# Kernel tuning notes

Measured on AMD Instinct MI355X. Metric: run time of the kernel, lower is better.

The kernel has to match this reference:

```python
import jax, jax.numpy as jnp
import numpy as np

N, E, DIN, H, EIN, EH, STEPS = 10000, 100000, 64, 64, 16, 128, 3


def setup_inputs() -> dict:
    key = jax.random.key(0)
    ks = jax.random.split(key, 8)
    n_feat = jax.random.normal(ks[0], (N, DIN), jnp.float32)
    e_feat = jax.random.normal(ks[1], (E, EIN), jnp.float32)
    src = jax.random.randint(ks[2], (E,), 0, N, jnp.int32)
    dst = jax.random.randint(ks[3], (E,), 0, N, jnp.int32)
    W0 = jax.random.normal(ks[4], (DIN, H), jnp.float32) / np.sqrt(DIN)
    b0 = jnp.zeros((H,), jnp.float32)
    We1 = jax.random.normal(ks[5], (EIN, EH), jnp.float32) / np.sqrt(EIN)
    be1 = jnp.zeros((EH,), jnp.float32)
    # small scale so per-edge HxH weight matrices keep activations stable
    We2 = jax.random.normal(ks[6], (EH, H * H), jnp.float32) * 0.02
    be2 = jnp.zeros((H * H,), jnp.float32)
    conv_bias = jnp.zeros((H,), jnp.float32)
    gamma = jnp.ones((H,), jnp.float32)
    beta = jnp.zeros((H,), jnp.float32)
    return {"n_feat": n_feat, "e_feat": e_feat, "src": src, "dst": dst,
            "W0": W0, "b0": b0, "We1": We1, "be1": be1, "We2": We2,
            "be2": be2, "conv_bias": conv_bias, "gamma": gamma, "beta": beta}


def reference(n_feat, e_feat, src, dst, W0, b0, We1, be1, We2, be2, conv_bias, gamma, beta):
    n = n_feat.shape[0]
    h = W0.shape[1]
    out = jax.nn.relu(n_feat @ W0 + b0)  # [N,H]
    # edge network (eval mode: dropout = identity); e_feat is fixed so the
    # per-edge weight matrices are identical each step -> compute once.
    w_edge = (jax.nn.relu(e_feat @ We1 + be1) @ We2 + be2).reshape(-1, h, h)  # [E,H,H]
    for _ in range(STEPS):
        msg = jnp.einsum('ei,eio->eo', out[src], w_edge)  # gather + per-edge matmul
        agg = jax.ops.segment_sum(msg, dst, num_segments=n)  # scatter-sum to dst
        out = jax.nn.relu(agg + conv_bias)
    # BatchNorm1d over nodes (training-mode batch statistics)
    mean = jnp.mean(out, axis=0)
    var = jnp.var(out, axis=0)
    return (out - mean) * jax.lax.rsqrt(var + 1e-5) * gamma + beta
```

## Files before the change

### kernel.cpp

```cpp
#include <hip/hip_runtime.h>
#include <stdint.h>

#define DIN   64
#define HDIM  64
#define EIN   16
#define EHID  128
#define HH    4096
#define TC    8256
#define STEPS 3

typedef short bf16x8 __attribute__((ext_vector_type(8)));
typedef float f32x4  __attribute__((ext_vector_type(4)));

__device__ __forceinline__ unsigned short f32_to_bf16(float f) {
    union { float f; uint32_t u; } v; v.f = f;
    uint32_t r = v.u + 0x7fffu + ((v.u >> 16) & 1u);
    return (unsigned short)(r >> 16);
}
__device__ __forceinline__ float bfu_to_f(unsigned short u) {
    union { uint32_t u; float f; } v; v.u = (uint32_t)u << 16; return v.f;
}

__global__ void k_node_mlp(const float* __restrict__ nf, const float* __restrict__ W0,
                           const float* __restrict__ b0, float* __restrict__ outb,
                           unsigned short* __restrict__ outbf, int n_nodes) {
    __shared__ float w0s[DIN * HDIM];
    int tid = threadIdx.x;
    for (int i = tid; i < DIN * HDIM; i += 256) w0s[i] = W0[i];
    __syncthreads();
    int node = blockIdx.x * 4 + (tid >> 6);
    int o = tid & 63;
    if (node >= n_nodes) return;
    float xr = nf[node * DIN + o];
    float acc = b0[o];
#pragma unroll 8
    for (int i = 0; i < DIN; ++i)
        acc += __shfl(xr, i, 64) * w0s[i * HDIM + o];
    float v = fmaxf(acc, 0.f);
    outb[node * HDIM + o] = v;
    outbf[node * HDIM + o] = f32_to_bf16(v);
}

__global__ void k_edge_mlp(const float* __restrict__ ef, const float* __restrict__ We1,
                           const float* __restrict__ be1, unsigned short* __restrict__ h, int n_edges) {
    int tid = threadIdx.x;
    int e = blockIdx.x * 2 + (tid >> 7);
    int c = tid & 127;
    if (e >= n_edges) return;
    float acc = be1[c];
    const float* x = ef + (size_t)e * EIN;
#pragma unroll
    for (int i = 0; i < EIN; ++i) acc += x[i] * We1[i * EHID + c];
    h[(size_t)e * EHID + c] = f32_to_bf16(fmaxf(acc, 0.f));
}

__global__ void k_bmat(const float* __restrict__ We2, const float* __restrict__ be2,
                       unsigned short* __restrict__ BmatT) {
    int t = blockIdx.x * 256 + threadIdx.x;
    if (t >= TC * 64) return;
    int c = t >> 6, i = t & 63;
    int g = c & 63;
    int m = (c & ~63) + 4 * (g & 15) + (g >> 4);
    float v;
    if (m < 8192) {
        int k = ((m >> 11) << 5) | (m & 31);
        int o = (m >> 5) & 63;
        v = We2[k * HH + i * 64 + o];
    } else {
        v = be2[i * 64 + (m - 8192)];
    }
    BmatT[t] = f32_to_bf16(v);
}

__global__ void k_T(const unsigned short* __restrict__ outbf, const unsigned short* __restrict__ BmatT,
                    unsigned short* __restrict__ T, int n0, int n1) {
    int wave = threadIdx.x >> 6, lane = threadIdx.x & 63;
    int r = lane & 15, q = lane >> 4;
    int eb = n0 + blockIdx.y * 64;
    int cb = blockIdx.x * 256 + wave * 64;
    f32x4 acc[4][4] = {};
#pragma unroll
    for (int s = 0; s < 2; ++s) {
        bf16x8 afr[4], bfr[4];
#pragma unroll
        for (int mt = 0; mt < 4; ++mt) {
            int e = eb + mt * 16 + r;
            if (e >= n1) e = n1 - 1;
            afr[mt] = *(const bf16x8*)(outbf + (size_t)e * 64 + s * 32 + q * 8);
        }
#pragma unroll
        for (int nt = 0; nt < 4; ++nt) {
            int c = cb + nt * 16 + r;
            if (c >= TC) c = 0;
            bfr[nt] = *(const bf16x8*)(BmatT + (size_t)c * 64 + s * 32 + q * 8);
        }
#pragma unroll
        for (int mt = 0; mt < 4; ++mt)
#pragma unroll
            for (int nt = 0; nt < 4; ++nt)
                acc[mt][nt] = __builtin_amdgcn_mfma_f32_16x16x32_bf16(afr[mt], bfr[nt], acc[mt][nt], 0, 0, 0);
    }
    if (cb >= TC) return;
#pragma unroll
    for (int mt = 0; mt < 4; ++mt)
#pragma unroll
        for (int rg = 0; rg < 4; ++rg) {
            int n = eb + mt * 16 + q * 4 + rg;
            if (n >= n1) continue;
            ushort4 pk;
            pk.x = f32_to_bf16(acc[mt][0][rg]);
            pk.y = f32_to_bf16(acc[mt][1][rg]);
            pk.z = f32_to_bf16(acc[mt][2][rg]);
            pk.w = f32_to_bf16(acc[mt][3][rg]);
            *(ushort4*)(T + (size_t)(n - n0) * TC + cb + 4 * r) = pk;
        }
}

__global__ void k_hist(const int* __restrict__ src, const int* __restrict__ dst,
                       int* __restrict__ cntS, int* __restrict__ cntD, int n_edges) {
    int e = blockIdx.x * 256 + threadIdx.x;
    if (e >= n_edges) return;
    atomicAdd(&cntS[src[e]], 1);
    atomicAdd(&cntD[dst[e]], 1);
}

__global__ void k_scan(const int* __restrict__ cntS, const int* __restrict__ cntD,
                       int* __restrict__ offS, int* __restrict__ offD,
                       int* __restrict__ curS, int* __restrict__ curD, int n, int total) {
    const int* cnt = blockIdx.x ? cntD : cntS;
    int* off = blockIdx.x ? offD : offS;
    int* cur = blockIdx.x ? curD : curS;
    __shared__ int part[256];
    int tid = threadIdx.x;
    int chunk = (n + 255) / 256;
    int c0 = tid * chunk, c1 = c0 + chunk; if (c1 > n) c1 = n; if (c0 > n) c0 = n;
    int s = 0;
    for (int i = c0; i < c1; ++i) s += cnt[i];
    part[tid] = s;
    __syncthreads();
    for (int st = 1; st < 256; st <<= 1) {
        int v = (tid >= st) ? part[tid - st] : 0;
        __syncthreads();
        part[tid] += v;
        __syncthreads();
    }
    int run = tid ? part[tid - 1] : 0;
    for (int i = c0; i < c1; ++i) { off[i] = run; cur[i] = run; run += cnt[i]; }
    if (tid == 0) off[n] = total;
}

__global__ void k_perm(const int* __restrict__ src, const int* __restrict__ dst,
                       int* __restrict__ curS, int* __restrict__ curD,
                       int* __restrict__ permS, int* __restrict__ permD, int n_edges) {
    int e = blockIdx.x * 256 + threadIdx.x;
    if (e >= n_edges) return;
    permS[atomicAdd(&curS[src[e]], 1)] = e;
    permD[atomicAdd(&curD[dst[e]], 1)] = e;
}

__global__ void k_msg(const unsigned short* __restrict__ h, const unsigned short* __restrict__ T,
                      const int* __restrict__ offS, const int* __restrict__ permS,
                      float* __restrict__ msg, int n0, int n1) {
    int wave = threadIdx.x >> 6, lane = threadIdx.x & 63;
    int n = n0 + blockIdx.x * 4 + wave;
    if (n >= n1) return;
    int beg = offS[n], end = offS[n + 1];
    if (beg == end) return;
    int r = lane & 15, q = lane >> 4;
    const unsigned short* Tb = T + (size_t)(n - n0) * TC;
    float bias[4];
#pragma unroll
    for (int nt = 0; nt < 4; ++nt)
        bias[nt] = bfu_to_f(Tb[8192 + nt * 16 + r]);
    for (int j0 = beg; j0 < end; j0 += 16) {
        int jc = j0 + r; if (jc >= end) jc = end - 1;
        int e = permS[jc];
        const unsigned short* he = h + (size_t)e * EHID;
        f32x4 acc[4] = {};
#pragma unroll
        for (int s = 0; s < 4; ++s) {
            bf16x8 afr = *(const bf16x8*)(he + s * 32 + q * 8);
#pragma unroll
            for (int nt = 0; nt < 4; ++nt) {
                bf16x8 bfr = *(const bf16x8*)(Tb + s * 2048 + (nt * 16 + r) * 32 + q * 8);
                acc[nt] = __builtin_amdgcn_mfma_f32_16x16x32_bf16(afr, bfr, acc[nt], 0, 0, 0);
            }
        }
#pragma unroll
        for (int rg = 0; rg < 4; ++rg) {
            int jr = j0 + q * 4 + rg;
            if (jr >= end) continue;
            int er = permS[jr];
#pragma unroll
            for (int nt = 0; nt < 4; ++nt)
                msg[(size_t)er * 64 + nt * 16 + r] = acc[nt][rg] + bias[nt];
        }
    }
}

__global__ void k_agg(const float* __restrict__ msg, const int* __restrict__ offD,
                      const int* __restrict__ permD, const float* __restrict__ cbias,
                      float* __restrict__ outb, unsigned short* __restrict__ outbf, int n_nodes) {
    int wave = threadIdx.x >> 6, lane = threadIdx.x & 63;
    int d = blockIdx.x * 4 + wave;
    if (d >= n_nodes) return;
    float acc = 0.f;
    int end = offD[d + 1];
    for (int j = offD[d]; j < end; ++j)
        acc += msg[(size_t)permD[j] * 64 + lane];
    float v = fmaxf(acc + cbias[lane], 0.f);
    outb[(size_t)d * 64 + lane] = v;
    outbf[(size_t)d * 64 + lane] = f32_to_bf16(v);
}

__global__ void k_bn_stats(const float* __restrict__ out, float* __restrict__ stat, int n_nodes) {
    __shared__ float s1[256], s2[256];
    int tid = threadIdx.x;
    int f = tid & 63, g = tid >> 6;
    float sum = 0.f, ss = 0.f;
    for (int r = blockIdx.x * 4 + g; r < n_nodes; r += 256) {
        float v = out[r * HDIM + f];
        sum += v; ss += v * v;
    }
    s1[tid] = sum; s2[tid] = ss;
    __syncthreads();
    if (tid < 64) {
        float A = s1[tid] + s1[64 + tid] + s1[128 + tid] + s1[192 + tid];
        float B = s2[tid] + s2[64 + tid] + s2[128 + tid] + s2[192 + tid];
        atomicAdd(&stat[tid], A);
        atomicAdd(&stat[64 + tid], B);
    }
}

__global__ void k_bn_final(const float* __restrict__ stat, const float* __restrict__ gamma,
                           const float* __restrict__ beta, float* __restrict__ sc, int n_nodes) {
    int f = threadIdx.x;
    if (f >= 64) return;
    float mean = stat[f] / n_nodes;
    float var  = stat[64 + f] / n_nodes - mean * mean;
    float inv  = rsqrtf(var + 1e-5f);
    float scale = gamma[f] * inv;
    sc[f] = scale;
    sc[64 + f] = beta[f] - mean * scale;
}

__global__ void k_bn_apply(const float* __restrict__ out, const float* __restrict__ sc,
                           float* __restrict__ y, int n) {
    int t = blockIdx.x * 256 + threadIdx.x;
    if (t >= n) return;
    int f = t & 63;
    y[t] = out[t] * sc[f] + sc[64 + f];
}

extern "C" void kernel_launch(void* const* d_in, const int* in_sizes, int n_in,
                              void* d_out, int out_size, void* d_ws, size_t ws_size,
                              hipStream_t stream) {
    const float* nf    = (const float*)d_in[0];
    const float* ef    = (const float*)d_in[1];
    const int*   src   = (const int*)d_in[2];
    const int*   dst   = (const int*)d_in[3];
    const float* W0    = (const float*)d_in[4];
    const float* b0    = (const float*)d_in[5];
    const float* We1   = (const float*)d_in[6];
    const float* be1   = (const float*)d_in[7];
    const float* We2   = (const float*)d_in[8];
    const float* be2   = (const float*)d_in[9];
    const float* cbias = (const float*)d_in[10];
    const float* gamma = (const float*)d_in[11];
    const float* beta  = (const float*)d_in[12];
    (void)n_in; (void)out_size;

    int n_nodes = in_sizes[0] / DIN;
    int n_edges = in_sizes[2];

    char* ws = (char*)d_ws;
    size_t off = 0;
    auto carve = [&](size_t bytes) -> void* {
        void* p = ws + off;
        off = (off + bytes + 255) & ~(size_t)255;
        return p;
    };
    unsigned short* h     = (unsigned short*)carve((size_t)n_edges * EHID * 2);
    float*          msg   = (float*)carve((size_t)n_edges * 64 * 4);
    float*          outb  = (float*)carve((size_t)n_nodes * HDIM * 4);
    unsigned short* outbf = (unsigned short*)carve((size_t)n_nodes * HDIM * 2);
    unsigned short* BmatT = (unsigned short*)carve((size_t)TC * 64 * 2);
    int*            offS  = (int*)carve((size_t)(n_nodes + 1) * 4);
    int*            offD  = (int*)carve((size_t)(n_nodes + 1) * 4);
    int*            curS  = (int*)carve((size_t)n_nodes * 4);
    int*            curD  = (int*)carve((size_t)n_nodes * 4);
    int*            permS = (int*)carve((size_t)n_edges * 4);
    int*            permD = (int*)carve((size_t)n_edges * 4);
    float*          stat  = (float*)carve(128 * 4 + (size_t)2 * n_nodes * 4);
    int*            cntS  = (int*)(stat + 128);
    int*            cntD  = cntS + n_nodes;
    float*          sc    = (float*)carve(128 * 4);
    unsigned short* T     = (unsigned short*)(ws + off);
    size_t avail = ws_size > off ? ws_size - off : 0;
    long tcap = (long)(avail / ((size_t)TC * 2));
    if (tcap > n_nodes) tcap = n_nodes;
    if (tcap < 64) tcap = 64;

    hipMemsetAsync(stat, 0, 128 * 4 + (size_t)2 * n_nodes * 4, stream);

    k_node_mlp<<<dim3((n_nodes + 3) / 4), 256, 0, stream>>>(nf, W0, b0, outb, outbf, n_nodes);
    k_edge_mlp<<<dim3((n_edges + 1) / 2), 256, 0, stream>>>(ef, We1, be1, h, n_edges);
    k_bmat<<<dim3((TC * 64 + 255) / 256), 256, 0, stream>>>(We2, be2, BmatT);
    k_hist<<<dim3((n_edges + 255) / 256), 256, 0, stream>>>(src, dst, cntS, cntD, n_edges);
    k_scan<<<dim3(2), 256, 0, stream>>>(cntS, cntD, offS, offD, curS, curD, n_nodes, n_edges);
    k_perm<<<dim3((n_edges + 255) / 256), 256, 0, stream>>>(src, dst, curS, curD, permS, permD, n_edges);

    for (int step = 0; step < STEPS; ++step) {
        for (long n0 = 0; n0 < n_nodes; n0 += tcap) {
            long n1 = n0 + tcap; if (n1 > n_nodes) n1 = n_nodes;
            long cnt = n1 - n0;
            k_T<<<dim3((TC + 255) / 256, (cnt + 63) / 64), 256, 0, stream>>>(
                outbf, BmatT, T, (int)n0, (int)n1);
            k_msg<<<dim3((cnt + 3) / 4), 256, 0, stream>>>(
                h, T, offS, permS, msg, (int)n0, (int)n1);
        }
        k_agg<<<dim3((n_nodes + 3) / 4), 256, 0, stream>>>(msg, offD, permD, cbias, outb, outbf, n_nodes);
    }

    k_bn_stats<<<dim3(64), 256, 0, stream>>>(outb, stat, n_nodes);
    k_bn_final<<<dim3(1), 64, 0, stream>>>(stat, gamma, beta, sc, n_nodes);
    k_bn_apply<<<dim3((n_nodes * HDIM + 255) / 256), 256, 0, stream>>>(
        outb, sc, (float*)d_out, n_nodes * HDIM);
}
```

Measured before the change: 509.1 us.

## Fuse per-node T computation and message MFMA into one LDS-resident kernel

Adds a k_step kernel. Each 512-thread block computes the per-node transformed weight rows T for 8 nodes into LDS (about 132 KB) and then runs the per-edge message MFMA directly from LDS. This removes the global write and re-read of the large T buffer (N x 8256 bf16) and the chunked launches. It runs only if the runtime accepts that dynamic LDS size, and it wastes half of each MFMA's rows because only 8 of 16 A rows are real nodes. The edge MLP is also rewritten to stage weights and inputs in shared memory and to emit packed 16-byte stores.

```diff
diff --git a/kernel.cpp b/kernel.cpp
--- a/kernel.cpp
+++ b/kernel.cpp
@@ -8,6 +8,8 @@
 #define HH    4096
 #define TC    8256
 #define STEPS 3
+#define G8    8
+#define LDS_BYTES (G8 * TC * 2)
 
 typedef short bf16x8 __attribute__((ext_vector_type(8)));
 typedef float f32x4  __attribute__((ext_vector_type(4)));
@@ -43,15 +45,32 @@
 
 __global__ void k_edge_mlp(const float* __restrict__ ef, const float* __restrict__ We1,
                            const float* __restrict__ be1, unsigned short* __restrict__ h, int n_edges) {
-    int tid = threadIdx.x;
-    int e = blockIdx.x * 2 + (tid >> 7);
-    int c = tid & 127;
-    if (e >= n_edges) return;
-    float acc = be1[c];
-    const float* x = ef + (size_t)e * EIN;
-#pragma unroll
-    for (int i = 0; i < EIN; ++i) acc += x[i] * We1[i * EHID + c];
-    h[(size_t)e * EHID + c] = f32_to_bf16(fmaxf(acc, 0.f));
+    __shared__ float w1s[EIN * EHID];
+    __shared__ float xs[16 * EIN];
+    int t = threadIdx.x;
+    int e0 = blockIdx.x * 16;
+#pragma unroll
+    for (int i = t; i < EIN * EHID; i += 256) w1s[i] = We1[i];
+    xs[t] = ef[(size_t)e0 * EIN + t];
+    __syncthreads();
+    int g = t >> 4, c0 = (t & 15) * 8;
+    int edge = e0 + g;
+    if (edge >= n_edges) return;
+    float acc[8];
+#pragma unroll
+    for (int j = 0; j < 8; ++j) acc[j] = be1[c0 + j];
+#pragma unroll
+    for (int i = 0; i < EIN; ++i) {
+        float xi = xs[g * EIN + i];
+#pragma unroll
+        for (int j = 0; j < 8; ++j) acc[j] += xi * w1s[i * EHID + c0 + j];
+    }
+    uint32_t p0 = f32_to_bf16(fmaxf(acc[0], 0.f)) | ((uint32_t)f32_to_bf16(fmaxf(acc[1], 0.f)) << 16);
+    uint32_t p1 = f32_to_bf16(fmaxf(acc[2], 0.f)) | ((uint32_t)f32_to_bf16(fmaxf(acc[3], 0.f)) << 16);
+    uint32_t p2 = f32_to_bf16(fmaxf(acc[4], 0.f)) | ((uint32_t)f32_to_bf16(fmaxf(acc[5], 0.f)) << 16);
+    uint32_t p3 = f32_to_bf16(fmaxf(acc[6], 0.f)) | ((uint32_t)f32_to_bf16(fmaxf(acc[7], 0.f)) << 16);
+    uint4 pk = {p0, p1, p2, p3};
+    *(uint4*)(h + (size_t)edge * EHID + c0) = pk;
 }
 
 __global__ void k_bmat(const float* __restrict__ We2, const float* __restrict__ be2,
@@ -72,6 +91,81 @@
     BmatT[t] = f32_to_bf16(v);
 }
 
+__global__ __launch_bounds__(512) void k_step(const unsigned short* __restrict__ outbf,
+                       const unsigned short* __restrict__ BmatT,
+                       const unsigned short* __restrict__ h,
+                       const int* __restrict__ offS, const int* __restrict__ permS,
+                       float* __restrict__ msg, int n_nodes) {
+    extern __shared__ unsigned short lds_T[];
+    int wave = threadIdx.x >> 6, lane = threadIdx.x & 63;
+    int r = lane & 15, q = lane >> 4;
+    int nb = blockIdx.x * G8;
+    {
+        int ga = nb + (r < G8 ? r : G8 - 1);
+        if (ga >= n_nodes) ga = n_nodes - 1;
+        bf16x8 afr0 = *(const bf16x8*)(outbf + (size_t)ga * 64 + q * 8);
+        bf16x8 afr1 = *(const bf16x8*)(outbf + (size_t)ga * 64 + 32 + q * 8);
+        for (int gi = wave; gi < TC / 64; gi += 8) {
+            int cb = gi * 64;
+            f32x4 acc[4] = {};
+#pragma unroll
+            for (int nt = 0; nt < 4; ++nt) {
+                size_t cofs = (size_t)(cb + nt * 16 + r) * 64;
+                bf16x8 b0 = *(const bf16x8*)(BmatT + cofs + q * 8);
+                bf16x8 b1 = *(const bf16x8*)(BmatT + cofs + 32 + q * 8);
+                acc[nt] = __builtin_amdgcn_mfma_f32_16x16x32_bf16(afr0, b0, acc[nt], 0, 0, 0);
+                acc[nt] = __builtin_amdgcn_mfma_f32_16x16x32_bf16(afr1, b1, acc[nt], 0, 0, 0);
+            }
+            if (q < 2) {
+#pragma unroll
+                for (int rg = 0; rg < 4; ++rg) {
+                    int g = q * 4 + rg;
+                    ushort4 pk;
+                    pk.x = f32_to_bf16(acc[0][rg]);
+                    pk.y = f32_to_bf16(acc[1][rg]);
+                    pk.z = f32_to_bf16(acc[2][rg]);
+                    pk.w = f32_to_bf16(acc[3][rg]);
+                    *(ushort4*)(lds_T + (size_t)g * TC + cb + 4 * r) = pk;
+                }
+            }
+        }
+    }
+    __syncthreads();
+    int n = nb + wave;
+    if (n >= n_nodes) return;
+    int beg = offS[n], end = offS[n + 1];
+    if (beg == end) return;
+    const unsigned short* Tb = lds_T + (size_t)wave * TC;
+    float bias[4];
+#pragma unroll
+    for (int nt = 0; nt < 4; ++nt)
+        bias[nt] = bfu_to_f(Tb[8192 + nt * 16 + r]);
+    for (int j0 = beg; j0 < end; j0 += 16) {
+        int jc = j0 + r; if (jc >= end) jc = end - 1;
+        int e = permS[jc];
+        const unsigned short* he = h + (size_t)e * EHID;
+        f32x4 acc[4] = {};
+#pragma unroll
+        for (int s = 0; s < 4; ++s) {
+            bf16x8 afr = *(const bf16x8*)(he + s * 32 + q * 8);
+#pragma unroll
+            for (int nt = 0; nt < 4; ++nt) {
+                bf16x8 bfr = *(const bf16x8*)(Tb + s * 2048 + (nt * 16 + r) * 32 + q * 8);
+                acc[nt] = __builtin_amdgcn_mfma_f32_16x16x32_bf16(afr, bfr, acc[nt], 0, 0, 0);
+            }
+        }
+#pragma unroll
+        for (int rg = 0; rg < 4; ++rg) {
+            int jr = j0 + q * 4 + rg;
+            if (jr >= end) continue;
+            int er = permS[jr];
+#pragma unroll
+            for (int nt = 0; nt < 4; ++nt)
+                msg[(size_t)er * 64 + nt * 16 + r] = acc[nt][rg] + bias[nt];
+        }
+    }
+}
+
 __global__ void k_T(const unsigned short* __restrict__ outbf, const unsigned short* __restrict__ BmatT,
                     unsigned short* __restrict__ T, int n0, int n1) {
     int wave = threadIdx.x >> 6, lane = threadIdx.x & 63;
@@ -114,6 +208,46 @@
             pk.w = f32_to_bf16(acc[mt][3][rg]);
             *(ushort4*)(T + (size_t)(n - n0) * TC + cb + 4 * r) = pk;
         }
+}
+
+__global__ void k_msg(const unsigned short* __restrict__ h, const unsigned short* __restrict__ T,
+                      const int* __restrict__ offS, const int* __restrict__ permS,
+                      float* __restrict__ msg, int n0, int n1) {
+    int wave = threadIdx.x >> 6, lane = threadIdx.x & 63;
+    int n = n0 + blockIdx.x * 4 + wave;
+    if (n >= n1) return;
+    int beg = offS[n], end = offS[n + 1];
+    if (beg == end) return;
+    int r = lane & 15, q = lane >> 4;
+    const unsigned short* Tb = T + (size_t)(n - n0) * TC;
+    float bias[4];
+#pragma unroll
+    for (int nt = 0; nt < 4; ++nt)
+        bias[nt] = bfu_to_f(Tb[8192 + nt * 16 + r]);
+    for (int j0 = beg; j0 < end; j0 += 16) {
+        int jc = j0 + r; if (jc >= end) jc = end - 1;
+        int e = permS[jc];
+        const unsigned short* he = h + (size_t)e * EHID;
+        f32x4 acc[4] = {};
+#pragma unroll
+        for (int s = 0; s < 4; ++s) {
+            bf16x8 afr = *(const bf16x8*)(he + s * 32 + q * 8);
+#pragma unroll
+            for (int nt = 0; nt < 4; ++nt) {
+                bf16x8 bfr = *(const bf16x8*)(Tb + s * 2048 + (nt * 16 + r) * 32 + q * 8);
+                acc[nt] = __builtin_amdgcn_mfma_f32_16x16x32_bf16(afr, bfr, acc[nt], 0, 0, 0);
+            }
+        }
+#pragma unroll
+        for (int rg = 0; rg < 4; ++rg) {
+            int jr = j0 + q * 4 + rg;
+            if (jr >= end) continue;
+            int er = permS[jr];
+#pragma unroll
+            for (int nt = 0; nt < 4; ++nt)
+                msg[(size_t)er * 64 + nt * 16 + r] = acc[nt][rg] + bias[nt];
+        }
+    }
 }
 
 __global__ void k_hist(const int* __restrict__ src, const int* __restrict__ dst,
@@ -156,46 +290,6 @@
     if (e >= n_edges) return;
     permS[atomicAdd(&curS[src[e]], 1)] = e;
     permD[atomicAdd(&curD[dst[e]], 1)] = e;
-}
-
-__global__ void k_msg(const unsigned short* __restrict__ h, const unsigned short* __restrict__ T,
-                      const int* __restrict__ offS, const int* __restrict__ permS,
-                      float* __restrict__ msg, int n0, int n1) {
-    int wave = threadIdx.x >> 6, lane = threadIdx.x & 63;
-    int n = n0 + blockIdx.x * 4 + wave;
-    if (n >= n1) return;
-    int beg = offS[n], end = offS[n + 1];
-    if (beg == end) return;
-    int r = lane & 15, q = lane >> 4;
-    const unsigned short* Tb = T + (size_t)(n - n0) * TC;
-    float bias[4];
-#pragma unroll
-    for (int nt = 0; nt < 4; ++nt)
-        bias[nt] = bfu_to_f(Tb[8192 + nt * 16 + r]);
-    for (int j0 = beg; j0 < end; j0 += 16) {
-        int jc = j0 + r; if (jc >= end) jc = end - 1;
-        int e = permS[jc];
-        const unsigned short* he = h + (size_t)e * EHID;
-        f32x4 acc[4] = {};
-#pragma unroll
-        for (int s = 0; s < 4; ++s) {
-            bf16x8 afr = *(const bf16x8*)(he + s * 32 + q * 8);
-#pragma unroll
-            for (int nt = 0; nt < 4; ++nt) {
-                bf16x8 bfr = *(const bf16x8*)(Tb + s * 2048 + (nt * 16 + r) * 32 + q * 8);
-                acc[nt] = __builtin_amdgcn_mfma_f32_16x16x32_bf16(afr, bfr, acc[nt], 0, 0, 0);
-            }
-        }
-#pragma unroll
-        for (int rg = 0; rg < 4; ++rg) {
-            int jr = j0 + q * 4 + rg;
-            if (jr >= end) continue;
-            int er = permS[jr];
-#pragma unroll
-            for (int nt = 0; nt < 4; ++nt)
-                msg[(size_t)er * 64 + nt * 16 + r] = acc[nt][rg] + bias[nt];
-        }
-    }
 }
 
 __global__ void k_agg(const float* __restrict__ msg, const int* __restrict__ offD,
@@ -301,23 +395,37 @@
     if (tcap > n_nodes) tcap = n_nodes;
     if (tcap < 64) tcap = 64;
 
+    bool fused = false;
+    if (hipFuncSetAttribute((const void*)k_step, hipFuncAttributeMaxDynamicSharedMemorySize,
+                            LDS_BYTES) == hipSuccess) {
+        hipFuncAttributes fa;
+        if (hipFuncGetAttributes(&fa, (const void*)k_step) == hipSuccess &&
+            fa.maxDynamicSharedSizeBytes >= LDS_BYTES)
+            fused = true;
+    }
+
     hipMemsetAsync(stat, 0, 128 * 4 + (size_t)2 * n_nodes * 4, stream);
 
     k_node_mlp<<<dim3((n_nodes + 3) / 4), 256, 0, stream>>>(nf, W0, b0, outb, outbf, n_nodes);
-    k_edge_mlp<<<dim3((n_edges + 1) / 2), 256, 0, stream>>>(ef, We1, be1, h, n_edges);
+    k_edge_mlp<<<dim3((n_edges + 15) / 16), 256, 0, stream>>>(ef, We1, be1, h, n_edges);
     k_bmat<<<dim3((TC * 64 + 255) / 256), 256, 0, stream>>>(We2, be2, BmatT);
     k_hist<<<dim3((n_edges + 255) / 256), 256, 0, stream>>>(src, dst, cntS, cntD, n_edges);
     k_scan<<<dim3(2), 256, 0, stream>>>(cntS, cntD, offS, offD, curS, curD, n_nodes, n_edges);
     k_perm<<<dim3((n_edges + 255) / 256), 256, 0, stream>>>(src, dst, curS, curD, permS, permD, n_edges);
 
     for (int step = 0; step < STEPS; ++step) {
-        for (long n0 = 0; n0 < n_nodes; n0 += tcap) {
-            long n1 = n0 + tcap; if (n1 > n_nodes) n1 = n_nodes;
-            long cnt = n1 - n0;
-            k_T<<<dim3((TC + 255) / 256, (cnt + 63) / 64), 256, 0, stream>>>(
-                outbf, BmatT, T, (int)n0, (int)n1);
-            k_msg<<<dim3((cnt + 3) / 4), 256, 0, stream>>>(
-                h, T, offS, permS, msg, (int)n0, (int)n1);
+        if (fused) {
+            k_step<<<dim3((n_nodes + G8 - 1) / G8), 512, LDS_BYTES, stream>>>(
+                outbf, BmatT, h, offS, permS, msg, n_nodes);
+        } else {
+            for (long n0 = 0; n0 < n_nodes; n0 += tcap) {
+                long n1 = n0 + tcap; if (n1 > n_nodes) n1 = n_nodes;
+                long cnt = n1 - n0;
+                k_T<<<dim3((TC + 255) / 256, (cnt + 63) / 64), 256, 0, stream>>>(
+                    outbf, BmatT, T, (int)n0, (int)n1);
+                k_msg<<<dim3((cnt + 3) / 4), 256, 0, stream>>>(
+                    h, T, offS, permS, msg, (int)n0, (int)n1);
+            }
         }
         k_agg<<<dim3((n_nodes + 3) / 4), 256, 0, stream>>>(msg, offD, permD, cbias, outb, outbf, n_nodes);
     }
```

Measured after the change: 718.7 us. 1.41x slower.
